# Kernel tuning notes

Hardware: AMD Instinct MI355X
Metric: run time of the kernel (lower is better)

## Reference

```python
import jax, jax.numpy as jnp
import numpy as np

N_NODES = 50000
N_EDGES = 800000
IN_CH, HID, HEADS, OUT_CH = 16, 64, 4, 8
NEG_SLOPE = 0.2


def _add_self_loops(edge_index, num_nodes):
    loop = jnp.arange(num_nodes, dtype=edge_index.dtype)
    loops = jnp.stack([loop, loop])  # [2, N]
    return jnp.concatenate([edge_index, loops], axis=1)


def _gat_conv(x, src, dst, W, a_src, a_dst, bias, concat):
    """PyG-style GATConv: linear -> per-edge LeakyReLU attention -> segment
    softmax over incoming edges -> scatter-add aggregate."""
    N = x.shape[0]
    H, C = a_src.shape
    h = (x @ W).reshape(N, H, C)                      # [N,H,C]
    alpha_src = (h * a_src).sum(-1)                   # [N,H]
    alpha_dst = (h * a_dst).sum(-1)                   # [N,H]
    e = jax.nn.leaky_relu(alpha_src[src] + alpha_dst[dst], NEG_SLOPE)  # [E,H]
    # numerically stable segment softmax over edges grouped by dst
    e_max = jax.ops.segment_max(e, dst, num_segments=N)
    e_exp = jnp.exp(e - e_max[dst])
    denom = jax.ops.segment_sum(e_exp, dst, num_segments=N)
    alpha = e_exp / denom[dst]                        # [E,H]
    msg = h[src] * alpha[:, :, None]                  # [E,H,C]
    out = jax.ops.segment_sum(msg, dst, num_segments=N)  # [N,H,C]
    if concat:
        return out.reshape(N, H * C) + bias
    return out.mean(axis=1) + bias


def setup_inputs() -> dict:
    key = jax.random.key(0)
    ks = jax.random.split(key, 12)
    s = 0.1
    return {
        "x": jax.random.normal(ks[0], (N_NODES, IN_CH), jnp.float32),
        "edge_index": jax.random.randint(ks[1], (2, N_EDGES), 0, N_NODES, jnp.int64),
        "W1": jax.random.normal(ks[2], (IN_CH, HEADS * HID), jnp.float32) * s,
        "as1": jax.random.normal(ks[3], (HEADS, HID), jnp.float32) * s,
        "ad1": jax.random.normal(ks[4], (HEADS, HID), jnp.float32) * s,
        "b1": jnp.zeros((HEADS * HID,), jnp.float32),
        "W2": jax.random.normal(ks[5], (HEADS * HID, HEADS * HID), jnp.float32) * s,
        "as2": jax.random.normal(ks[6], (HEADS, HID), jnp.float32) * s,
        "ad2": jax.random.normal(ks[7], (HEADS, HID), jnp.float32) * s,
        "b2": jnp.zeros((HID,), jnp.float32),
        "Wc": jax.random.normal(ks[8], (HID, OUT_CH), jnp.float32) * s,
        "bc": jnp.zeros((OUT_CH,), jnp.float32),
    }


def reference(x, edge_index, W1, as1, ad1, b1, W2, as2, ad2, b2, Wc, bc):
    ei = _add_self_loops(edge_index, x.shape[0])
    src, dst = ei[0], ei[1]
    h = _gat_conv(x, src, dst, W1, as1, ad1, b1, concat=True)
    h = jax.nn.elu(h)
    h = _gat_conv(h, src, dst, W2, as2, ad2, b2, concat=False)
    h = jax.nn.elu(h)
    return h @ Wc + bc  # [N, OUT_CH]
```

## Files before the change

### kernel.cpp

```cpp
#include <hip/hip_runtime.h>
#include <math.h>

#define NODES   50000
#define HEADS   4
#define HID     64
#define FDIM    256
#define IN_CH   16
#define NEG_SLOPE 0.2f

typedef unsigned short ushort_t;
typedef unsigned int uint_t;
typedef __attribute__((ext_vector_type(8))) short bf16x8;
typedef __attribute__((ext_vector_type(4))) float f32x4;
typedef __attribute__((ext_vector_type(4))) uint_t u32x4;

__device__ inline ushort_t f2bf(float f) {
    uint_t u = __float_as_uint(f);
    u += 0x7fffu + ((u >> 16) & 1u);
    return (ushort_t)(u >> 16);
}
__device__ inline uint_t f2h(float f) {
    _Float16 h = (_Float16)f;
    return (uint_t)*(ushort_t*)&h;
}
__device__ inline float h2f(uint_t u) {
    ushort_t us = (ushort_t)u;
    _Float16 h = *(_Float16*)&us;
    return (float)h;
}

__device__ inline void fmamix8(float* a, uint4 hv, float pw) {
    asm("v_fma_mix_f32 %0, %8, %9, %0 op_sel:[0,0,0] op_sel_hi:[0,1,0]\n\t"
        "v_fma_mix_f32 %1, %8, %9, %1 op_sel:[0,1,0] op_sel_hi:[0,1,0]\n\t"
        "v_fma_mix_f32 %2, %8, %10, %2 op_sel:[0,0,0] op_sel_hi:[0,1,0]\n\t"
        "v_fma_mix_f32 %3, %8, %10, %3 op_sel:[0,1,0] op_sel_hi:[0,1,0]\n\t"
        "v_fma_mix_f32 %4, %8, %11, %4 op_sel:[0,0,0] op_sel_hi:[0,1,0]\n\t"
        "v_fma_mix_f32 %5, %8, %11, %5 op_sel:[0,1,0] op_sel_hi:[0,1,0]\n\t"
        "v_fma_mix_f32 %6, %8, %12, %6 op_sel:[0,0,0] op_sel_hi:[0,1,0]\n\t"
        "v_fma_mix_f32 %7, %8, %12, %7 op_sel:[0,1,0] op_sel_hi:[0,1,0]"
        : "+v"(a[0]), "+v"(a[1]), "+v"(a[2]), "+v"(a[3]),
          "+v"(a[4]), "+v"(a[5]), "+v"(a[6]), "+v"(a[7])
        : "v"(pw), "v"(hv.x), "v"(hv.y), "v"(hv.z), "v"(hv.w));
}


__global__ __launch_bounds__(256) void k_prep(const float* __restrict__ x,
                                              const float* __restrict__ W1,
                                              const float* __restrict__ as1,
                                              const float* __restrict__ ad1,
                                              const float* __restrict__ W2,
                                              const int* __restrict__ ei, int E,
                                              ushort_t* __restrict__ h,
                                              float* __restrict__ asrc,
                                              float* __restrict__ adst,
                                              ushort_t* __restrict__ W2T,
                                              int* __restrict__ deg, int Nn, int NB) {
    __shared__ float2 sred[8][256];
    int bid = blockIdx.x, t = threadIdx.x;
    if (bid >= NB + 256) {
        int e = (bid - NB - 256) * 256 + t;
        int Etot = E + Nn;
        if (e >= Etot) return;
        int d = (e < E) ? ei[E + e] : (e - E);
        if (d >= 0 && d < Nn) atomicAdd(&deg[d], 1);
        return;
    }
    if (bid >= NB) {
        int idx = (bid - NB) * 256 + t;
        int n = idx >> 8, k = idx & 255;
        W2T[idx] = f2bf(W2[k * FDIM + n]);
        return;
    }
    float w1c[16];
#pragma unroll
    for (int k = 0; k < 16; ++k) w1c[k] = W1[k * FDIM + t];
    float av = as1[t], dv = ad1[t];
    int hh = t >> 6;
#pragma unroll
    for (int j = 0; j < 8; ++j) {
        int n = bid * 8 + j;
        const float4* xp = (const float4*)(x + n * IN_CH);
        float4 x0 = xp[0], x1 = xp[1], x2 = xp[2], x3 = xp[3];
        float s = x0.x * w1c[0]  + x0.y * w1c[1]  + x0.z * w1c[2]  + x0.w * w1c[3]
                + x1.x * w1c[4]  + x1.y * w1c[5]  + x1.z * w1c[6]  + x1.w * w1c[7]
                + x2.x * w1c[8]  + x2.y * w1c[9]  + x2.z * w1c[10] + x2.w * w1c[11]
                + x3.x * w1c[12] + x3.y * w1c[13] + x3.z * w1c[14] + x3.w * w1c[15];
        uint_t pv = f2h(s);
        uint_t ov = __shfl_down(pv, 1);
        if (!(t & 1))
            *(uint_t*)(h + (((long)hh * Nn + n) << 6) + (t & 63)) = pv | (ov << 16);
        sred[j][t] = make_float2(s * av, s * dv);
    }
    __syncthreads();
    int o = t >> 3, q = t & 7;
    int jj = o >> 2, h2 = o & 3;
    float2 r = make_float2(0.f, 0.f);
#pragma unroll
    for (int i = 0; i < 8; ++i) {
        float2 v = sred[jj][h2 * 64 + q * 8 + i];
        r.x += v.x; r.y += v.y;
    }
#pragma unroll
    for (int m = 1; m < 8; m <<= 1) {
        r.x += __shfl_xor(r.x, m);
        r.y += __shfl_xor(r.y, m);
    }
    if (q == 0) {
        int n = bid * 8 + jj;
        asrc[n * 4 + h2] = r.x;
        adst[n * 4 + h2] = r.y;
    }
}


__global__ __launch_bounds__(256) void k_scanA(const int* __restrict__ deg,
                                               int* __restrict__ bsum, int N) {
    __shared__ int sh[256];
    int t = threadIdx.x;
    int i0 = blockIdx.x * 4096 + t * 16;
    int s = 0;
#pragma unroll
    for (int j = 0; j < 16; ++j) s += (i0 + j < N) ? deg[i0 + j] : 0;
    sh[t] = s;
    __syncthreads();
    for (int off = 128; off; off >>= 1) {
        if (t < off) sh[t] += sh[t + off];
        __syncthreads();
    }
    if (t == 0) bsum[blockIdx.x] = sh[0];
}

__global__ void k_scanB(int* __restrict__ bsum, int* __restrict__ rowst, int nb, int N) {
    int t = threadIdx.x;
    int orig = (t < nb) ? bsum[t] : 0;
    int v = orig;
#pragma unroll
    for (int off = 1; off < 64; off <<= 1) {
        int u = __shfl_up(v, off);
        if (t >= off) v += u;
    }
    if (t < nb) bsum[t] = v - orig;
    if (t == 63) rowst[N] = v;
}

__global__ __launch_bounds__(256) void k_scanC(const int* __restrict__ deg,
                                               const int* __restrict__ bsum,
                                               int* __restrict__ rowst,
                                               int* __restrict__ cursor, int N) {
    __shared__ int sh[256];
    int t = threadIdx.x, b = blockIdx.x;
    int i0 = b * 4096 + t * 16;
    int v[16], s = 0;
#pragma unroll
    for (int j = 0; j < 16; ++j) { v[j] = (i0 + j < N) ? deg[i0 + j] : 0; s += v[j]; }
    sh[t] = s;
    __syncthreads();
    for (int off = 1; off < 256; off <<= 1) {
        int u = (t >= off) ? sh[t - off] : 0;
        __syncthreads();
        sh[t] += u;
        __syncthreads();
    }
    int excl = sh[t] - s + bsum[b];
#pragma unroll
    for (int j = 0; j < 16; ++j) {
        if (i0 + j < N) { rowst[i0 + j] = excl; cursor[i0 + j] = excl; }
        excl += v[j];
    }
}

__global__ void k_scatter(const int* __restrict__ ei, int E, int N,
                          int* __restrict__ cursor, int2* __restrict__ csr2) {
    int e = blockIdx.x * blockDim.x + threadIdx.x;
    int Etot = E + N;
    if (e >= Etot) return;
    int s, d;
    if (e < E) { s = ei[e]; d = ei[E + e]; } else { s = d = e - E; }
    if (d < 0 || d >= N) return;
    int pos = atomicAdd(&cursor[d], 1);
    csr2[pos] = make_int2(s, d);
}


__global__ __launch_bounds__(256) void k_gemm2(const ushort_t* __restrict__ A,
                                               const ushort_t* __restrict__ BT,
                                               const float* __restrict__ as2,
                                               const float* __restrict__ ad2,
                                               ushort_t* __restrict__ C,
                                               float* __restrict__ asrc,
                                               float* __restrict__ adst, int M) {
    __shared__ short As[64 * 40];
    __shared__ short Bs[64 * 40];
    __shared__ float2 red[64][2];
    int tid = threadIdx.x;
    int row0 = blockIdx.y * 64, col0 = blockIdx.x * 64;
    int wid = tid >> 6, lane = tid & 63;
    int wm = wid >> 1, wn = wid & 1;
    int quad = lane >> 4, lm = lane & 15;
    int lr = tid >> 2, lk = (tid & 3) * 8;
    f32x4 acc[2][2] = {};
    for (int k0 = 0; k0 < FDIM; k0 += 32) {
        uint4 av = {0u, 0u, 0u, 0u};
        int ar = row0 + lr;
        if (ar < M) av = *(const uint4*)(A + (long)ar * FDIM + k0 + lk);
        *(uint4*)(&As[lr * 40 + lk]) = av;
        uint4 bv = *(const uint4*)(BT + (long)(col0 + lr) * FDIM + k0 + lk);
        *(uint4*)(&Bs[lr * 40 + lk]) = bv;
        __syncthreads();
        bf16x8 a0 = *(const bf16x8*)(&As[(wm * 32 + lm) * 40 + quad * 8]);
        bf16x8 a1 = *(const bf16x8*)(&As[(wm * 32 + 16 + lm) * 40 + quad * 8]);
        bf16x8 b0 = *(const bf16x8*)(&Bs[(wn * 32 + lm) * 40 + quad * 8]);
        bf16x8 b1 = *(const bf16x8*)(&Bs[(wn * 32 + 16 + lm) * 40 + quad * 8]);
        acc[0][0] = __builtin_amdgcn_mfma_f32_16x16x32_bf16(a0, b0, acc[0][0], 0, 0, 0);
        acc[0][1] = __builtin_amdgcn_mfma_f32_16x16x32_bf16(a0, b1, acc[0][1], 0, 0, 0);
        acc[1][0] = __builtin_amdgcn_mfma_f32_16x16x32_bf16(a1, b0, acc[1][0], 0, 0, 0);
        acc[1][1] = __builtin_amdgcn_mfma_f32_16x16x32_bf16(a1, b1, acc[1][1], 0, 0, 0);
        __syncthreads();
    }
#pragma unroll
    for (int mi = 0; mi < 2; ++mi)
#pragma unroll
        for (int ni = 0; ni < 2; ++ni)
#pragma unroll
            for (int r = 0; r < 4; ++r) {
                int row = row0 + wm * 32 + mi * 16 + quad * 4 + r;
                int colw = wn * 32 + ni * 16 + lm;
                if (row < M)
                    C[(((long)blockIdx.x * M + row) << 6) + colw] = (ushort_t)f2h(acc[mi][ni][r]);
            }
    float asv0 = as2[col0 + wn * 32 + lm], asv1 = as2[col0 + wn * 32 + 16 + lm];
    float adv0 = ad2[col0 + wn * 32 + lm], adv1 = ad2[col0 + wn * 32 + 16 + lm];
#pragma unroll
    for (int mi = 0; mi < 2; ++mi)
#pragma unroll
        for (int r = 0; r < 4; ++r) {
            float ps = acc[mi][0][r] * asv0 + acc[mi][1][r] * asv1;
            float pd = acc[mi][0][r] * adv0 + acc[mi][1][r] * adv1;
#pragma unroll
            for (int off = 1; off < 16; off <<= 1) {
                ps += __shfl_xor(ps, off);
                pd += __shfl_xor(pd, off);
            }
            if (lm == 0) red[wm * 32 + mi * 16 + quad * 4 + r][wn] = make_float2(ps, pd);
        }
    __syncthreads();
    if (tid < 64) {
        int row = row0 + tid;
        if (row < M) {
            float2 e0 = red[tid][0], e1 = red[tid][1];
            asrc[row * 4 + blockIdx.x] = e0.x + e1.x;
            adst[row * 4 + blockIdx.x] = e0.y + e1.y;
        }
    }
}


__global__ void k_pw(const int2* __restrict__ csr2, const float* __restrict__ asrc,
                     const float* __restrict__ adst, uint_t* __restrict__ pwb, int Etot) {
    int e = blockIdx.x * blockDim.x + threadIdx.x;
    if (e >= Etot) return;
    int2 sd = csr2[e];
    float4 av = *(const float4*)(asrc + sd.x * 4);
    float4 dv = *(const float4*)(adst + sd.y * 4);
    float t[4] = {av.x + dv.x, av.y + dv.y, av.z + dv.z, av.w + dv.w};
    uint_t sh = (uint_t)sd.x << 16;
#pragma unroll
    for (int h = 0; h < 4; ++h) {
        float tt = (t[h] > 0.f) ? t[h] : NEG_SLOPE * t[h];
        pwb[h * Etot + e] = sh | f2h(__expf(tt));
    }
}


__global__ __launch_bounds__(256) void k_agg(const ushort_t* __restrict__ h,
                                             const uint_t* __restrict__ pwb,
                                             const int* __restrict__ row_start,
                                             const float* __restrict__ b1,
                                             ushort_t* __restrict__ hout,
                                             ushort_t* __restrict__ zn,
                                             int mode, int Etot, int N) {
    int tid  = threadIdx.x;
    int bid  = blockIdx.x;
    int head = bid & 3;
    int nb   = bid >> 2;
    int wv   = tid >> 6;
    int lane = tid & 63;
    int half = lane >> 5;
    int l32  = lane & 31;
    int g    = l32 >> 3;
    int cg   = l32 & 7;
    int d    = nb * 8 + wv * 2 + half;
    bool valid = d < N;

    int s0 = 0, s1 = 0;
    if (valid) { s0 = row_start[d]; s1 = row_start[d + 1]; }
    int cnt  = s1 - s0;
    int maxc = max(cnt, __shfl_xor(cnt, 32));

    const char* hb  = (const char*)h + ((size_t)head * (size_t)N << 7);
    const char* pwc = (const char*)pwb;
    uint_t loff  = (uint_t)cg * 16;
    uint_t pbyte = ((uint_t)head * (uint_t)Etot + (uint_t)(s0 + g)) << 2;

    float acc[8] = {0.f, 0.f, 0.f, 0.f, 0.f, 0.f, 0.f, 0.f};
    float den = 0.f;

    for (int off = 0; off < maxc; off += 16) {
        int i0 = s0 + off + g;
        uint_t pb = pbyte + ((uint_t)off << 2);
        uint_t u0 = __builtin_nontemporal_load((const uint_t*)(pwc + pb));
        uint_t u1 = __builtin_nontemporal_load((const uint_t*)(pwc + pb + 16));
        uint_t u2 = __builtin_nontemporal_load((const uint_t*)(pwc + pb + 32));
        uint_t u3 = __builtin_nontemporal_load((const uint_t*)(pwc + pb + 48));
        uint4 hv0 = *(const uint4*)(hb + (((u0 >> 16) << 7) + loff));
        uint4 hv1 = *(const uint4*)(hb + (((u1 >> 16) << 7) + loff));
        uint4 hv2 = *(const uint4*)(hb + (((u2 >> 16) << 7) + loff));
        uint4 hv3 = *(const uint4*)(hb + (((u3 >> 16) << 7) + loff));
        float pw0 = (i0      < s1) ? h2f(u0 & 0xffffu) : 0.f;
        float pw1 = (i0 + 4  < s1) ? h2f(u1 & 0xffffu) : 0.f;
        float pw2 = (i0 + 8  < s1) ? h2f(u2 & 0xffffu) : 0.f;
        float pw3 = (i0 + 12 < s1) ? h2f(u3 & 0xffffu) : 0.f;
        den += (pw0 + pw1) + (pw2 + pw3);
        fmamix8(acc, hv0, pw0);
        fmamix8(acc, hv1, pw1);
        fmamix8(acc, hv2, pw2);
        fmamix8(acc, hv3, pw3);
    }
#pragma unroll
    for (int off = 8; off <= 16; off <<= 1) {
#pragma unroll
        for (int j = 0; j < 8; ++j) acc[j] += __shfl_xor(acc[j], off);
        den += __shfl_xor(den, off);
    }

    if (g != 0 || !valid) return;
    float inv = 1.f / den;
    if (mode) {
        const float* bp = b1 + head * HID + cg * 8;
        float v[8];
#pragma unroll
        for (int j = 0; j < 8; ++j) {
            float t = acc[j] * inv + bp[j];
            v[j] = (t > 0.f) ? t : __expf(t) - 1.f;
        }
        u32x4 u;
        u.x = (uint_t)f2bf(v[0]) | ((uint_t)f2bf(v[1]) << 16);
        u.y = (uint_t)f2bf(v[2]) | ((uint_t)f2bf(v[3]) << 16);
        u.z = (uint_t)f2bf(v[4]) | ((uint_t)f2bf(v[5]) << 16);
        u.w = (uint_t)f2bf(v[6]) | ((uint_t)f2bf(v[7]) << 16);
        __builtin_nontemporal_store(u, (u32x4*)(hout + (long)d * FDIM + head * HID + cg * 8));
    } else {
        u32x4 u;
        u.x = f2h(acc[0] * inv) | (f2h(acc[1] * inv) << 16);
        u.y = f2h(acc[2] * inv) | (f2h(acc[3] * inv) << 16);
        u.z = f2h(acc[4] * inv) | (f2h(acc[5] * inv) << 16);
        u.w = f2h(acc[6] * inv) | (f2h(acc[7] * inv) << 16);
        __builtin_nontemporal_store(u, (u32x4*)(zn + (((long)head * N + d) << 6) + cg * 8));
    }
}


__global__ __launch_bounds__(256) void k_fin(const ushort_t* __restrict__ zn,
                                             const float* __restrict__ b2,
                                             const float* __restrict__ Wc,
                                             const float* __restrict__ bc,
                                             float* __restrict__ out, int N) {
    __shared__ float zsh[256];
    __shared__ float wsh[584];
    int tid = threadIdx.x;
    for (int i = tid; i < 584; i += 256)
        wsh[i] = (i < 512) ? Wc[i] : ((i < 520) ? bc[i - 512] : b2[i - 520]);
    __syncthreads();
    int ln = tid >> 6, c = tid & 63;
    int n = blockIdx.x * 4 + ln;
    if (n < N) {
        long base = ((long)n << 6) + c;
        long hs = (long)N << 6;
        float v = 0.25f * (h2f(zn[base]) + h2f(zn[base + hs])
                         + h2f(zn[base + 2 * hs]) + h2f(zn[base + 3 * hs]))
                + wsh[520 + c];
        zsh[ln * 64 + c] = (v > 0.f) ? v : __expf(v) - 1.f;
    }
    __syncthreads();
    if (tid < 32) {
        int ln2 = tid >> 3, o = tid & 7;
        int nn = blockIdx.x * 4 + ln2;
        if (nn < N) {
            float acc = wsh[512 + o];
            const float* zp = zsh + ln2 * 64;
#pragma unroll 8
            for (int c2 = 0; c2 < 64; ++c2) acc += zp[c2] * wsh[c2 * 8 + o];
            out[(long)nn * 8 + o] = acc;
        }
    }
}


extern "C" void kernel_launch(void* const* d_in, const int* in_sizes, int n_in,
                              void* d_out, int out_size, void* d_ws, size_t ws_size,
                              hipStream_t stream) {
    const float* x   = (const float*)d_in[0];
    const int*   ei  = (const int*)d_in[1];
    const float* W1  = (const float*)d_in[2];
    const float* as1 = (const float*)d_in[3];
    const float* ad1 = (const float*)d_in[4];
    const float* b1  = (const float*)d_in[5];
    const float* W2  = (const float*)d_in[6];
    const float* as2 = (const float*)d_in[7];
    const float* ad2 = (const float*)d_in[8];
    const float* b2  = (const float*)d_in[9];
    const float* Wc  = (const float*)d_in[10];
    const float* bc  = (const float*)d_in[11];
    float* out = (float*)d_out;

    const int N = NODES;
    const int E = in_sizes[1] / 2;
    const int Etot = E + N;

    char* ws = (char*)d_ws;
    size_t off = 0;
    auto alloc = [&](size_t bytes) {
        void* p = ws + off;
        off = (off + bytes + 255) & ~(size_t)255;
        return p;
    };
    ushort_t* hbf    = (ushort_t*)alloc((size_t)N * FDIM * 2);
    ushort_t* hact   = (ushort_t*)alloc((size_t)N * FDIM * 2);
    float*    asrc   = (float*)alloc((size_t)N * HEADS * 4);
    float*    adst   = (float*)alloc((size_t)N * HEADS * 4);
    ushort_t* W2T    = (ushort_t*)alloc((size_t)FDIM * FDIM * 2);
    int*      deg    = (int*)alloc((size_t)N * 4);
    int*      rowst  = (int*)alloc((size_t)(N + 1) * 4);
    int*      cursor = (int*)alloc((size_t)N * 4);
    int*      bsum   = (int*)alloc(64 * 4);
    int2*     csr2   = (int2*)alloc((size_t)Etot * 8);
    uint_t*   pwb    = (uint_t*)alloc((size_t)Etot * HEADS * 4 + 256);
    ushort_t* znorm  = hact;

    const int tpb = 256;
    int egrid = (Etot + tpb - 1) / tpb;
    int nb = (N + 4095) / 4096;
    int NB = (N + 7) / 8;
    int agrid = 4 * ((N + 7) / 8);

    hipMemsetAsync(deg, 0, (size_t)N * 4, stream);

    k_prep<<<NB + 256 + egrid, tpb, 0, stream>>>(x, W1, as1, ad1, W2, ei, E,
                                                 hbf, asrc, adst, W2T, deg, N, NB);
    k_scanA<<<nb, 256, 0, stream>>>(deg, bsum, N);
    k_scanB<<<1, 64, 0, stream>>>(bsum, rowst, nb, N);
    k_scanC<<<nb, 256, 0, stream>>>(deg, bsum, rowst, cursor, N);
    k_scatter<<<egrid, tpb, 0, stream>>>(ei, E, N, cursor, csr2);

    k_pw<<<egrid, tpb, 0, stream>>>(csr2, asrc, adst, pwb, Etot);
    k_agg<<<agrid, 256, 0, stream>>>(hbf, pwb, rowst, b1, hact, nullptr, 1, Etot, N);

    dim3 g2(FDIM / 64, (N + 63) / 64);
    k_gemm2<<<g2, 256, 0, stream>>>(hact, W2T, as2, ad2, hbf, asrc, adst, N);
    k_pw<<<egrid, tpb, 0, stream>>>(csr2, asrc, adst, pwb, Etot);
    k_agg<<<agrid, 256, 0, stream>>>(hbf, pwb, rowst, nullptr, nullptr, znorm, 0, Etot, N);
    k_fin<<<(N + 3) / 4, 256, 0, stream>>>(znorm, b2, Wc, bc, out, N);
}
```

Baseline: 374.4 us.

## Sort destination nodes by degree to balance aggregation half-wave workloads

```diff
diff --git a/kernel.cpp b/kernel.cpp
--- a/kernel.cpp
+++ b/kernel.cpp
@@ -114,39 +114,69 @@
 
 
 __global__ __launch_bounds__(256) void k_scanA(const int* __restrict__ deg,
-                                               int* __restrict__ bsum, int N) {
+                                               int* __restrict__ bsum,
+                                               int* __restrict__ dhist, int N) {
+    __shared__ int sh[256];
+    __shared__ int lh[256];
+    int t = threadIdx.x;
+    lh[t] = 0;
+    __syncthreads();
+    int i0 = blockIdx.x * 4096 + t * 16;
+    int s = 0;
+#pragma unroll
+    for (int j = 0; j < 16; ++j) {
+        if (i0 + j < N) {
+            int dv = deg[i0 + j];
+            s += dv;
+            int b = 255 - ((dv < 255) ? dv : 255);
+            atomicAdd(&lh[b], 1);
+        }
+    }
+    sh[t] = s;
+    __syncthreads();
+    for (int off = 128; off; off >>= 1) {
+        if (t < off) sh[t] += sh[t + off];
+        __syncthreads();
+    }
+    if (t == 0) bsum[blockIdx.x] = sh[0];
+    atomicAdd(&dhist[t], lh[t]);
+}
+
+__global__ __launch_bounds__(256) void k_scanB(int* __restrict__ bsum,
+                                               int* __restrict__ rowst,
+                                               const int* __restrict__ dhist,
+                                               int* __restrict__ dcur, int nb, int N) {
     __shared__ int sh[256];
     int t = threadIdx.x;
-    int i0 = blockIdx.x * 4096 + t * 16;
-    int s = 0;
-#pragma unroll
-    for (int j = 0; j < 16; ++j) s += (i0 + j < N) ? deg[i0 + j] : 0;
-    sh[t] = s;
-    __syncthreads();
-    for (int off = 128; off; off >>= 1) {
-        if (t < off) sh[t] += sh[t + off];
-        __syncthreads();
-    }
-    if (t == 0) bsum[blockIdx.x] = sh[0];
-}
-
-__global__ void k_scanB(int* __restrict__ bsum, int* __restrict__ rowst, int nb, int N) {
-    int t = threadIdx.x;
-    int orig = (t < nb) ? bsum[t] : 0;
-    int v = orig;
-#pragma unroll
-    for (int off = 1; off < 64; off <<= 1) {
-        int u = __shfl_up(v, off);
-        if (t >= off) v += u;
-    }
-    if (t < nb) bsum[t] = v - orig;
-    if (t == 63) rowst[N] = v;
+    if (t < 64) {
+        int orig = (t < nb) ? bsum[t] : 0;
+        int v = orig;
+#pragma unroll
+        for (int off = 1; off < 64; off <<= 1) {
+            int u = __shfl_up(v, off);
+            if (t >= off) v += u;
+        }
+        if (t < nb) bsum[t] = v - orig;
+        if (t == 63) rowst[N] = v;
+    }
+    int dv = dhist[t];
+    sh[t] = dv;
+    __syncthreads();
+    for (int off = 1; off < 256; off <<= 1) {
+        int u = (t >= off) ? sh[t - off] : 0;
+        __syncthreads();
+        sh[t] += u;
+        __syncthreads();
+    }
+    dcur[t] = sh[t] - dv;
 }
 
 __global__ __launch_bounds__(256) void k_scanC(const int* __restrict__ deg,
                                                const int* __restrict__ bsum,
                                                int* __restrict__ rowst,
-                                               int* __restrict__ cursor, int N) {
+                                               int* __restrict__ cursor,
+                                               int* __restrict__ dcur,
+                                               int* __restrict__ perm, int N) {
     __shared__ int sh[256];
     int t = threadIdx.x, b = blockIdx.x;
     int i0 = b * 4096 + t * 16;
@@ -164,7 +194,13 @@
     int excl = sh[t] - s + bsum[b];
 #pragma unroll
     for (int j = 0; j < 16; ++j) {
-        if (i0 + j < N) { rowst[i0 + j] = excl; cursor[i0 + j] = excl; }
+        if (i0 + j < N) {
+            rowst[i0 + j] = excl;
+            cursor[i0 + j] = excl;
+            int bin = 255 - ((v[j] < 255) ? v[j] : 255);
+            int pos = atomicAdd(&dcur[bin], 1);
+            perm[pos] = i0 + j;
+        }
         excl += v[j];
     }
 }
@@ -275,6 +311,7 @@
 __global__ __launch_bounds__(256) void k_agg(const ushort_t* __restrict__ h,
                                              const uint_t* __restrict__ pwb,
                                              const int* __restrict__ row_start,
+                                             const int* __restrict__ perm,
                                              const float* __restrict__ b1,
                                              ushort_t* __restrict__ hout,
                                              ushort_t* __restrict__ zn,
@@ -289,8 +326,9 @@
     int l32  = lane & 31;
     int g    = l32 >> 3;
     int cg   = l32 & 7;
-    int d    = nb * 8 + wv * 2 + half;
-    bool valid = d < N;
+    int idx  = nb * 8 + wv * 2 + half;
+    bool valid = idx < N;
+    int d    = valid ? perm[idx] : 0;
 
     int s0 = 0, s1 = 0;
     if (valid) { s0 = row_start[d]; s1 = row_start[d + 1]; }
@@ -433,6 +471,9 @@
     int*      rowst  = (int*)alloc((size_t)(N + 1) * 4);
     int*      cursor = (int*)alloc((size_t)N * 4);
     int*      bsum   = (int*)alloc(64 * 4);
+    int*      dhist  = (int*)alloc(256 * 4);
+    int*      dcur   = (int*)alloc(256 * 4);
+    int*      perm   = (int*)alloc((size_t)N * 4);
     int2*     csr2   = (int2*)alloc((size_t)Etot * 8);
     uint_t*   pwb    = (uint_t*)alloc((size_t)Etot * HEADS * 4 + 256);
     ushort_t* znorm  = hact;
@@ -444,20 +485,21 @@
     int agrid = 4 * ((N + 7) / 8);
 
     hipMemsetAsync(deg, 0, (size_t)N * 4, stream);
+    hipMemsetAsync(dhist, 0, 256 * 4, stream);
 
     k_prep<<<NB + 256 + egrid, tpb, 0, stream>>>(x, W1, as1, ad1, W2, ei, E,
                                                  hbf, asrc, adst, W2T, deg, N, NB);
-    k_scanA<<<nb, 256, 0, stream>>>(deg, bsum, N);
-    k_scanB<<<1, 64, 0, stream>>>(bsum, rowst, nb, N);
-    k_scanC<<<nb, 256, 0, stream>>>(deg, bsum, rowst, cursor, N);
+    k_scanA<<<nb, 256, 0, stream>>>(deg, bsum, dhist, N);
+    k_scanB<<<1, 256, 0, stream>>>(bsum, rowst, dhist, dcur, nb, N);
+    k_scanC<<<nb, 256, 0, stream>>>(deg, bsum, rowst, cursor, dcur, perm, N);
     k_scatter<<<egrid, tpb, 0, stream>>>(ei, E, N, cursor, csr2);
 
     k_pw<<<egrid, tpb, 0, stream>>>(csr2, asrc, adst, pwb, Etot);
-    k_agg<<<agrid, 256, 0, stream>>>(hbf, pwb, rowst, b1, hact, nullptr, 1, Etot, N);
+    k_agg<<<agrid, 256, 0, stream>>>(hbf, pwb, rowst, perm, b1, hact, nullptr, 1, Etot, N);
 
     dim3 g2(FDIM / 64, (N + 63) / 64);
     k_gemm2<<<g2, 256, 0, stream>>>(hact, W2T, as2, ad2, hbf, asrc, adst, N);
     k_pw<<<egrid, tpb, 0, stream>>>(csr2, asrc, adst, pwb, Etot);
-    k_agg<<<agrid, 256, 0, stream>>>(hbf, pwb, rowst, nullptr, nullptr, znorm, 0, Etot, N);
+    k_agg<<<agrid, 256, 0, stream>>>(hbf, pwb, rowst, perm, nullptr, nullptr, znorm, 0, Etot, N);
     k_fin<<<(N + 3) / 4, 256, 0, stream>>>(znorm, b2, Wc, bc, out, N);
 }
```

Result: slower. 527.6 us (+40.9%).

## Process four destination rows per half-wave with prefetched edge weights in k_agg

Applied to the files above, without the earlier changes.

```diff
diff --git a/kernel.cpp b/kernel.cpp
--- a/kernel.cpp
+++ b/kernel.cpp
@@ -289,73 +289,96 @@
     int l32  = lane & 31;
     int g    = l32 >> 3;
     int cg   = l32 & 7;
-    int d    = nb * 8 + wv * 2 + half;
-    bool valid = d < N;
-
-    int s0 = 0, s1 = 0;
-    if (valid) { s0 = row_start[d]; s1 = row_start[d + 1]; }
-    int cnt  = s1 - s0;
-    int maxc = max(cnt, __shfl_xor(cnt, 32));
+    int dbase = nb * 32 + wv * 8 + half;
 
     const char* hb  = (const char*)h + ((size_t)head * (size_t)N << 7);
     const char* pwc = (const char*)pwb;
-    uint_t loff  = (uint_t)cg * 16;
-    uint_t pbyte = ((uint_t)head * (uint_t)Etot + (uint_t)(s0 + g)) << 2;
-
-    float acc[8] = {0.f, 0.f, 0.f, 0.f, 0.f, 0.f, 0.f, 0.f};
-    float den = 0.f;
-
-    for (int off = 0; off < maxc; off += 16) {
-        int i0 = s0 + off + g;
-        uint_t pb = pbyte + ((uint_t)off << 2);
-        uint_t u0 = __builtin_nontemporal_load((const uint_t*)(pwc + pb));
-        uint_t u1 = __builtin_nontemporal_load((const uint_t*)(pwc + pb + 16));
-        uint_t u2 = __builtin_nontemporal_load((const uint_t*)(pwc + pb + 32));
-        uint_t u3 = __builtin_nontemporal_load((const uint_t*)(pwc + pb + 48));
-        uint4 hv0 = *(const uint4*)(hb + (((u0 >> 16) << 7) + loff));
-        uint4 hv1 = *(const uint4*)(hb + (((u1 >> 16) << 7) + loff));
-        uint4 hv2 = *(const uint4*)(hb + (((u2 >> 16) << 7) + loff));
-        uint4 hv3 = *(const uint4*)(hb + (((u3 >> 16) << 7) + loff));
-        float pw0 = (i0      < s1) ? h2f(u0 & 0xffffu) : 0.f;
-        float pw1 = (i0 + 4  < s1) ? h2f(u1 & 0xffffu) : 0.f;
-        float pw2 = (i0 + 8  < s1) ? h2f(u2 & 0xffffu) : 0.f;
-        float pw3 = (i0 + 12 < s1) ? h2f(u3 & 0xffffu) : 0.f;
-        den += (pw0 + pw1) + (pw2 + pw3);
-        fmamix8(acc, hv0, pw0);
-        fmamix8(acc, hv1, pw1);
-        fmamix8(acc, hv2, pw2);
-        fmamix8(acc, hv3, pw3);
-    }
-#pragma unroll
-    for (int off = 8; off <= 16; off <<= 1) {
-#pragma unroll
-        for (int j = 0; j < 8; ++j) acc[j] += __shfl_xor(acc[j], off);
-        den += __shfl_xor(den, off);
-    }
-
-    if (g != 0 || !valid) return;
-    float inv = 1.f / den;
-    if (mode) {
-        const float* bp = b1 + head * HID + cg * 8;
-        float v[8];
-#pragma unroll
-        for (int j = 0; j < 8; ++j) {
-            float t = acc[j] * inv + bp[j];
-            v[j] = (t > 0.f) ? t : __expf(t) - 1.f;
-        }
-        u32x4 u;
-        u.x = (uint_t)f2bf(v[0]) | ((uint_t)f2bf(v[1]) << 16);
-        u.y = (uint_t)f2bf(v[2]) | ((uint_t)f2bf(v[3]) << 16);
-        u.z = (uint_t)f2bf(v[4]) | ((uint_t)f2bf(v[5]) << 16);
-        u.w = (uint_t)f2bf(v[6]) | ((uint_t)f2bf(v[7]) << 16);
-        __builtin_nontemporal_store(u, (u32x4*)(hout + (long)d * FDIM + head * HID + cg * 8));
-    } else {
-        u32x4 u;
-        u.x = f2h(acc[0] * inv) | (f2h(acc[1] * inv) << 16);
-        u.y = f2h(acc[2] * inv) | (f2h(acc[3] * inv) << 16);
-        u.z = f2h(acc[4] * inv) | (f2h(acc[5] * inv) << 16);
-        u.w = f2h(acc[6] * inv) | (f2h(acc[7] * inv) << 16);
-        __builtin_nontemporal_store(u, (u32x4*)(zn + (((long)head * N + d) << 6) + cg * 8));
+    uint_t loff = (uint_t)cg * 16;
+    uint_t hoff = (uint_t)head * (uint_t)Etot;
+
+    int S0[4], S1[4];
+#pragma unroll
+    for (int k = 0; k < 4; ++k) {
+        int d  = dbase + k * 2;
+        int dc = (d < N) ? d : (N - 1);
+        S0[k] = row_start[dc];
+        S1[k] = (d < N) ? row_start[dc + 1] : S0[k];
+    }
+    uint_t PB[4];
+    uint_t U[4][4];
+#pragma unroll
+    for (int k = 0; k < 4; ++k) {
+        PB[k] = (hoff + (uint_t)(S0[k] + g)) << 2;
+#pragma unroll
+        for (int j = 0; j < 4; ++j)
+            U[k][j] = __builtin_nontemporal_load((const uint_t*)(pwc + PB[k] + (uint_t)j * 16u));
+    }
+
+#pragma unroll
+    for (int k = 0; k < 4; ++k) {
+        int d  = dbase + k * 2;
+        int s0 = S0[k], s1 = S1[k];
+        int cnt  = s1 - s0;
+        int maxc = max(cnt, __shfl_xor(cnt, 32));
+
+        float acc[8] = {0.f, 0.f, 0.f, 0.f, 0.f, 0.f, 0.f, 0.f};
+        float den = 0.f;
+        uint_t u0 = U[k][0], u1 = U[k][1], u2 = U[k][2], u3 = U[k][3];
+
+        for (int off = 0; off < maxc; off += 16) {
+            uint4 hv0 = *(const uint4*)(hb + (((u0 >> 16) << 7) + loff));
+            uint4 hv1 = *(const uint4*)(hb + (((u1 >> 16) << 7) + loff));
+            uint4 hv2 = *(const uint4*)(hb + (((u2 >> 16) << 7) + loff));
+            uint4 hv3 = *(const uint4*)(hb + (((u3 >> 16) << 7) + loff));
+            uint_t pb = PB[k] + ((uint_t)(off + 16) << 2);
+            uint_t n0 = __builtin_nontemporal_load((const uint_t*)(pwc + pb));
+            uint_t n1 = __builtin_nontemporal_load((const uint_t*)(pwc + pb + 16));
+            uint_t n2 = __builtin_nontemporal_load((const uint_t*)(pwc + pb + 32));
+            uint_t n3 = __builtin_nontemporal_load((const uint_t*)(pwc + pb + 48));
+            int i0 = s0 + off + g;
+            float pw0 = (i0      < s1) ? h2f(u0 & 0xffffu) : 0.f;
+            float pw1 = (i0 + 4  < s1) ? h2f(u1 & 0xffffu) : 0.f;
+            float pw2 = (i0 + 8  < s1) ? h2f(u2 & 0xffffu) : 0.f;
+            float pw3 = (i0 + 12 < s1) ? h2f(u3 & 0xffffu) : 0.f;
+            den += (pw0 + pw1) + (pw2 + pw3);
+            fmamix8(acc, hv0, pw0);
+            fmamix8(acc, hv1, pw1);
+            fmamix8(acc, hv2, pw2);
+            fmamix8(acc, hv3, pw3);
+            u0 = n0; u1 = n1; u2 = n2; u3 = n3;
+        }
+#pragma unroll
+        for (int off = 8; off <= 16; off <<= 1) {
+#pragma unroll
+            for (int j = 0; j < 8; ++j) acc[j] += __shfl_xor(acc[j], off);
+            den += __shfl_xor(den, off);
+        }
+
+        if (g == 0 && d < N) {
+            float inv = 1.f / den;
+            if (mode) {
+                const float* bp = b1 + head * HID + cg * 8;
+                float v[8];
+#pragma unroll
+                for (int j = 0; j < 8; ++j) {
+                    float t = acc[j] * inv + bp[j];
+                    v[j] = (t > 0.f) ? t : __expf(t) - 1.f;
+                }
+                u32x4 u;
+                u.x = (uint_t)f2bf(v[0]) | ((uint_t)f2bf(v[1]) << 16);
+                u.y = (uint_t)f2bf(v[2]) | ((uint_t)f2bf(v[3]) << 16);
+                u.z = (uint_t)f2bf(v[4]) | ((uint_t)f2bf(v[5]) << 16);
+                u.w = (uint_t)f2bf(v[6]) | ((uint_t)f2bf(v[7]) << 16);
+                __builtin_nontemporal_store(u, (u32x4*)(hout + (long)d * FDIM + head * HID + cg * 8));
+            } else {
+                u32x4 u;
+                u.x = f2h(acc[0] * inv) | (f2h(acc[1] * inv) << 16);
+                u.y = f2h(acc[2] * inv) | (f2h(acc[3] * inv) << 16);
+                u.z = f2h(acc[4] * inv) | (f2h(acc[5] * inv) << 16);
+                u.w = f2h(acc[6] * inv) | (f2h(acc[7] * inv) << 16);
+                __builtin_nontemporal_store(u, (u32x4*)(zn + (((long)head * N + d) << 6) + cg * 8));
+            }
+        }
     }
 }
 
@@ -365,7 +388,7 @@
                                              const float* __restrict__ Wc,
                                              const float* __restrict__ bc,
                                              float* __restrict__ out, int N) {
-    __shared__ float zsh[256];
+    __shared__ float zsh[4 * 65];
     __shared__ float wsh[584];
     int tid = threadIdx.x;
     for (int i = tid; i < 584; i += 256)
@@ -379,7 +402,7 @@
         float v = 0.25f * (h2f(zn[base]) + h2f(zn[base + hs])
                          + h2f(zn[base + 2 * hs]) + h2f(zn[base + 3 * hs]))
                 + wsh[520 + c];
-        zsh[ln * 64 + c] = (v > 0.f) ? v : __expf(v) - 1.f;
+        zsh[ln * 65 + c] = (v > 0.f) ? v : __expf(v) - 1.f;
     }
     __syncthreads();
     if (tid < 32) {
@@ -387,7 +410,7 @@
         int nn = blockIdx.x * 4 + ln2;
         if (nn < N) {
             float acc = wsh[512 + o];
-            const float* zp = zsh + ln2 * 64;
+            const float* zp = zsh + ln2 * 65;
 #pragma unroll 8
             for (int c2 = 0; c2 < 64; ++c2) acc += zp[c2] * wsh[c2 * 8 + o];
             out[(long)nn * 8 + o] = acc;
@@ -434,14 +457,14 @@
     int*      cursor = (int*)alloc((size_t)N * 4);
     int*      bsum   = (int*)alloc(64 * 4);
     int2*     csr2   = (int2*)alloc((size_t)Etot * 8);
-    uint_t*   pwb    = (uint_t*)alloc((size_t)Etot * HEADS * 4 + 256);
+    uint_t*   pwb    = (uint_t*)alloc((size_t)Etot * HEADS * 4 + 512);
     ushort_t* znorm  = hact;
 
     const int tpb = 256;
     int egrid = (Etot + tpb - 1) / tpb;
     int nb = (N + 4095) / 4096;
     int NB = (N + 7) / 8;
-    int agrid = 4 * ((N + 7) / 8);
+    int agrid = 4 * ((N + 31) / 32);
 
     hipMemsetAsync(deg, 0, (size_t)N * 4, stream);
 
```

After: 389.9 us. 4.1% more time.
